# Kernel optimization log

Hardware: AMD Instinct MI355X
Metric: run time of the kernel (lower is better)

Reference implementation:

```python
import jax, jax.numpy as jnp
import numpy as np

N, E = 50000, 800000
IN, HID, HEADS, OUT = 128, 32, 8, 40
D1 = HID * HEADS  # 256


def setup_inputs() -> dict:
    key = jax.random.key(0)
    ks = jax.random.split(key, 24)

    def w(k, fin, fout):
        return (jax.random.normal(k, (fin, fout), jnp.float32) / np.sqrt(fin)).astype(jnp.float32)

    def b(k, fout):
        return (jax.random.normal(k, (fout,), jnp.float32) * 0.02).astype(jnp.float32)

    inp = {
        "x": jax.random.normal(ks[0], (N, IN), jnp.float32),
        "edge_index": jax.random.randint(ks[1], (2, E), 0, N, dtype=jnp.int64),
        # layer 1: TransformerConv(IN -> HID, heads=HEADS, concat=True, beta=True)
        "q1w": w(ks[2], IN, D1), "q1b": b(ks[3], D1),
        "k1w": w(ks[4], IN, D1), "k1b": b(ks[5], D1),
        "v1w": w(ks[6], IN, D1), "v1b": b(ks[7], D1),
        "s1w": w(ks[8], IN, D1), "s1b": b(ks[9], D1),
        "b1w": w(ks[10], 3 * D1, 1),
        # layer 2: TransformerConv(D1 -> OUT, heads=1, concat=False, beta=True)
        "q2w": w(ks[11], D1, OUT), "q2b": b(ks[12], OUT),
        "k2w": w(ks[13], D1, OUT), "k2b": b(ks[14], OUT),
        "v2w": w(ks[15], D1, OUT), "v2b": b(ks[16], OUT),
        "s2w": w(ks[17], D1, OUT), "s2b": b(ks[18], OUT),
        "b2w": w(ks[19], 3 * OUT, 1),
    }
    return inp


def _tconv(x, src, dst, qw, qb, kw, kb, vw, vb, sw, sb, bw, heads, ch, concat):
    """PyG TransformerConv (no edge_attr, root_weight=True, beta=True), eval mode."""
    n = x.shape[0]
    q = (x @ qw + qb).reshape(n, heads, ch)
    k = (x @ kw + kb).reshape(n, heads, ch)
    v = (x @ vw + vb).reshape(n, heads, ch)
    # per-edge attention logits: message flows src(j) -> dst(i)
    alpha = jnp.einsum("ehc,ehc->eh", q[dst], k[src]) / np.sqrt(ch)  # [E,H]
    # segment softmax over incoming edges of each dst node
    amax = jax.ops.segment_max(alpha, dst, num_segments=n)  # [N,H]
    a = jnp.exp(alpha - amax[dst])
    asum = jax.ops.segment_sum(a, dst, num_segments=n)  # [N,H]
    attn = a / asum[dst]  # [E,H]
    # scatter-aggregate weighted values
    out = jax.ops.segment_sum(v[src] * attn[:, :, None], dst, num_segments=n)  # [N,H,C]
    out = out.reshape(n, heads * ch) if concat else out.mean(axis=1)
    skip = x @ sw + sb
    beta = jax.nn.sigmoid(jnp.concatenate([out, skip, out - skip], axis=-1) @ bw)  # [N,1]
    return beta * skip + (1.0 - beta) * out


def reference(x, edge_index, q1w, q1b, k1w, k1b, v1w, v1b, s1w, s1b, b1w,
              q2w, q2b, k2w, k2b, v2w, v2b, s2w, s2b, b2w):
    src, dst = edge_index[0], edge_index[1]
    h = jax.nn.elu(_tconv(x, src, dst, q1w, q1b, k1w, k1b, v1w, v1b, s1w, s1b, b1w, HEADS, HID, True))
    return _tconv(h, src, dst, q2w, q2b, k2w, k2b, v2w, v2b, s2w, s2b, b2w, 1, OUT, False)
```

## Files before the change

### kernel.cpp

```cpp
#include <hip/hip_runtime.h>
#include <cstdint>
#include <cstddef>

#define N_NODES 50000
#define N_EDGES 800000
#define IN_F    128
#define HID     32
#define HEADS   8
#define OUT_F   40
#define D1      256
#define W1COLS  1024
#define W2COLS  160
#define CAP     64

typedef unsigned short ushortT;
typedef unsigned char  ucharT;
typedef unsigned short ushortx8 __attribute__((ext_vector_type(8)));
typedef __bf16 bf16x8 __attribute__((ext_vector_type(8)));
typedef float floatx4 __attribute__((ext_vector_type(4)));
typedef float floatx2 __attribute__((ext_vector_type(2)));

__device__ inline ushortT f2bf(float f) {
    union { float f; unsigned int u; } c; c.f = f;
    unsigned int r = c.u + 0x7FFFu + ((c.u >> 16) & 1u);
    return (ushortT)(r >> 16);
}
__device__ inline float bf2f(ushortT h) {
    union { unsigned int u; float f; } c; c.u = ((unsigned int)h) << 16; return c.f;
}

#define PREP_FILL_B  3125
#define PREP_CONV_B  6250
#define PREP_W1_B    512
#define PREP_W2_B    160
#define PREP_TOTAL_B (PREP_FILL_B + PREP_CONV_B + PREP_W1_B + PREP_W2_B)

__global__ __launch_bounds__(256) void k_prep(
        const int* __restrict__ ei, int* __restrict__ cursor, int* __restrict__ col,
        const float* __restrict__ x, ushortT* __restrict__ xb,
        const float* __restrict__ q1w, const float* __restrict__ k1w,
        const float* __restrict__ v1w, const float* __restrict__ s1w,
        const float* __restrict__ q1b, const float* __restrict__ k1b,
        const float* __restrict__ v1b, const float* __restrict__ s1b,
        ushortT* __restrict__ W1T, float* __restrict__ b1c,
        const float* __restrict__ q2w, const float* __restrict__ k2w,
        const float* __restrict__ v2w, const float* __restrict__ s2w,
        const float* __restrict__ q2b, const float* __restrict__ k2b,
        const float* __restrict__ v2b, const float* __restrict__ s2b,
        ushortT* __restrict__ W2T, float* __restrict__ b2c) {
    int b = blockIdx.x;
    int tid = threadIdx.x;
    if (b < PREP_FILL_B) {
        int e = b * 256 + tid;
        if (e < N_EDGES) {
            int d = ei[N_EDGES + e];
            int p = atomicAdd(&cursor[d], 1);
            col[d * CAP + p] = ei[e];
        }
    } else if (b < PREP_FILL_B + PREP_CONV_B) {
        int i = (b - PREP_FILL_B) * 256 + tid;
        float4 v = reinterpret_cast<const float4*>(x)[i];
        ushort4 o;
        o.x = f2bf(v.x); o.y = f2bf(v.y); o.z = f2bf(v.z); o.w = f2bf(v.w);
        reinterpret_cast<ushort4*>(xb)[i] = o;
    } else if (b < PREP_FILL_B + PREP_CONV_B + PREP_W1_B) {
        int t = (b - PREP_FILL_B - PREP_CONV_B) * 256 + tid;
        int c = t / IN_F, k = t % IN_F;
        int sel = c >> 8, cc = c & 255;
        const float* w = sel == 0 ? q1w : sel == 1 ? k1w : sel == 2 ? v1w : s1w;
        W1T[(size_t)c * IN_F + k] = f2bf(w[(size_t)k * D1 + cc]);
        if (k == 0) {
            const float* bb = sel == 0 ? q1b : sel == 1 ? k1b : sel == 2 ? v1b : s1b;
            b1c[c] = bb[cc];
        }
    } else {
        int t = (b - PREP_FILL_B - PREP_CONV_B - PREP_W1_B) * 256 + tid;
        int c = t / D1, k = t % D1;
        int sel = c / OUT_F, cc = c % OUT_F;
        const float* w = sel == 0 ? q2w : sel == 1 ? k2w : sel == 2 ? v2w : s2w;
        W2T[(size_t)c * D1 + k] = f2bf(w[(size_t)k * OUT_F + cc]);
        if (k == 0) {
            const float* bb = sel == 0 ? q2b : sel == 1 ? k2b : sel == 2 ? v2b : s2b;
            b2c[c] = bb[cc];
        }
    }
}

template<int MODE>
__global__ __launch_bounds__(256) void gemm_mfma_pack(
        const ushortT* __restrict__ A, const ushortT* __restrict__ BT,
        const float* __restrict__ bias, float* __restrict__ QSf,
        ushortT* __restrict__ QSh, ucharT* __restrict__ KV8,
        ushortT* __restrict__ K2V2, int M, int K, int Nn) {
    constexpr int TM = 128, TN = 128, TK = 64, LDP = 72;
    __shared__ ushortT As[TM * LDP];
    __shared__ ushortT Bs[TN * LDP];
    int tid = threadIdx.x;
    int lane = tid & 63, wave = tid >> 6;
    int bm = blockIdx.x * TM, bn = blockIdx.y * TN;
    int wm = (wave & 1) * 64, wn = (wave >> 1) * 64;
    int mrow = lane & 15, g = lane >> 4;
    floatx4 acc[4][4] = {};

    for (int k0 = 0; k0 < K; k0 += TK) {
#pragma unroll
        for (int it = 0; it < 4; ++it) {
            int idx = tid + it * 256;
            int r = idx >> 3, c = (idx & 7) * 8;
            int gm = bm + r;
            ushortx8 val;
            if (gm < M) val = *reinterpret_cast<const ushortx8*>(A + (size_t)gm * K + k0 + c);
            else        val = (ushortx8)0;
            *reinterpret_cast<ushortx8*>(As + r * LDP + c) = val;
        }
#pragma unroll
        for (int it = 0; it < 4; ++it) {
            int idx = tid + it * 256;
            int r = idx >> 3, c = (idx & 7) * 8;
            int gn = bn + r;
            ushortx8 val;
            if (gn < Nn) val = *reinterpret_cast<const ushortx8*>(BT + (size_t)gn * K + k0 + c);
            else         val = (ushortx8)0;
            *reinterpret_cast<ushortx8*>(Bs + r * LDP + c) = val;
        }
        __syncthreads();
#pragma unroll
        for (int kc = 0; kc < TK / 32; ++kc) {
            bf16x8 a[4], b[4];
#pragma unroll
            for (int i = 0; i < 4; ++i)
                a[i] = *reinterpret_cast<const bf16x8*>(As + (wm + i * 16 + mrow) * LDP + kc * 32 + g * 8);
#pragma unroll
            for (int j = 0; j < 4; ++j)
                b[j] = *reinterpret_cast<const bf16x8*>(Bs + (wn + j * 16 + mrow) * LDP + kc * 32 + g * 8);
#pragma unroll
            for (int i = 0; i < 4; ++i)
#pragma unroll
                for (int j = 0; j < 4; ++j)
                    acc[i][j] = __builtin_amdgcn_mfma_f32_16x16x32_bf16(a[i], b[j], acc[i][j], 0, 0, 0);
        }
        __syncthreads();
    }

    if (MODE == 1) {
        float* lds = reinterpret_cast<float*>(As) + wave * 1088;
        int sec = blockIdx.y >> 1;
        int ccbase = (blockIdx.y & 1) * 128 + wn;
        int cb4 = (lane & 15) * 4;
        int rlo = lane >> 4;
        float4 bv = *reinterpret_cast<const float4*>(bias + blockIdx.y * 128 + wn + cb4);
#pragma unroll
        for (int i = 0; i < 4; ++i) {
#pragma unroll
            for (int j = 0; j < 4; ++j)
#pragma unroll
                for (int r = 0; r < 4; ++r)
                    lds[(g * 4 + r) * 68 + j * 16 + mrow] = acc[i][j][r];
#pragma unroll
            for (int it = 0; it < 4; ++it) {
                int row = it * 4 + rlo;
                int gm = bm + wm + i * 16 + row;
                if (gm >= M) continue;
                float4 v = *reinterpret_cast<float4*>(lds + row * 68 + cb4);
                v.x += bv.x; v.y += bv.y; v.z += bv.z; v.w += bv.w;
                int cc = ccbase + cb4;
                if (sec == 0 || sec == 3) {
                    ushort4 h;
                    h.x = f2bf(v.x); h.y = f2bf(v.y); h.z = f2bf(v.z); h.w = f2bf(v.w);
                    ushortT* dst = QSh + (size_t)gm * 512 + (sec == 3 ? 256 : 0) + cc;
                    *reinterpret_cast<ushort4*>(dst) = h;
                } else {
                    unsigned int pk = 0;
                    pk = __builtin_amdgcn_cvt_pk_fp8_f32(v.x, v.y, pk, false);
                    pk = __builtin_amdgcn_cvt_pk_fp8_f32(v.z, v.w, pk, true);
                    ucharT* dst = KV8 + (size_t)gm * 512 + (sec == 2 ? 256 : 0) + cc;
                    *reinterpret_cast<unsigned int*>(dst) = pk;
                }
            }
        }
    } else {
#pragma unroll
        for (int i = 0; i < 4; ++i) {
#pragma unroll
            for (int j = 0; j < 4; ++j) {
                int gn = bn + wn + j * 16 + mrow;
                if (gn >= Nn) continue;
                float bvs = bias[gn];
#pragma unroll
                for (int r = 0; r < 4; ++r) {
                    int gm = bm + wm + i * 16 + g * 4 + r;
                    if (gm >= M) continue;
                    float val = acc[i][j][r] + bvs;
                    int sec = gn / OUT_F, cc = gn % OUT_F;
                    if (sec == 0)      QSf[(size_t)gm * 80 + cc] = val;
                    else if (sec == 1) K2V2[(size_t)gm * 80 + cc] = f2bf(val);
                    else if (sec == 2) K2V2[(size_t)gm * 80 + 40 + cc] = f2bf(val);
                    else               QSf[(size_t)gm * 80 + 40 + cc] = val;
                }
            }
        }
    }
}

__global__ __launch_bounds__(256) void k_edge1(
        const ushortT* __restrict__ QSh, const ucharT* __restrict__ KV8,
        const float* __restrict__ bw,
        const int* __restrict__ degc, const int* __restrict__ col,
        ushortT* __restrict__ H1b) {
    int gid  = blockIdx.x * blockDim.x + threadIdx.x;
    int node = gid >> 6;
    int lane = threadIdx.x & 63;
    if (node >= N_NODES) return;
    const float scale = 0.17677669529663687f;
    ushort4 qh = *reinterpret_cast<const ushort4*>(QSh + (size_t)node * 512 + lane * 4);
    float4 q;
    q.x = bf2f(qh.x) * scale; q.y = bf2f(qh.y) * scale;
    q.z = bf2f(qh.z) * scale; q.w = bf2f(qh.w) * scale;

    float l = 0.f;
    float4 acc = make_float4(0.f, 0.f, 0.f, 0.f);
    int start = node * CAP;
    int d = degc[node];
    int t = 0;
    for (; t + 2 <= d; t += 2) {
        int j0 = col[start + t];
        int j1 = col[start + t + 1];
        const ucharT* row0 = KV8 + (size_t)j0 * 512 + lane * 4;
        const ucharT* row1 = KV8 + (size_t)j1 * 512 + lane * 4;
        unsigned int ku0 = *reinterpret_cast<const unsigned int*>(row0);
        unsigned int vu0 = *reinterpret_cast<const unsigned int*>(row0 + 256);
        unsigned int ku1 = *reinterpret_cast<const unsigned int*>(row1);
        unsigned int vu1 = *reinterpret_cast<const unsigned int*>(row1 + 256);
        floatx2 k0a = __builtin_amdgcn_cvt_pk_f32_fp8(ku0, false);
        floatx2 k0b = __builtin_amdgcn_cvt_pk_f32_fp8(ku0, true);
        floatx2 k1a = __builtin_amdgcn_cvt_pk_f32_fp8(ku1, false);
        floatx2 k1b = __builtin_amdgcn_cvt_pk_f32_fp8(ku1, true);
        float p0 = q.x * k0a[0] + q.y * k0a[1] + q.z * k0b[0] + q.w * k0b[1];
        float p1 = q.x * k1a[0] + q.y * k1a[1] + q.z * k1b[0] + q.w * k1b[1];
        p0 += __shfl_xor(p0, 1);  p1 += __shfl_xor(p1, 1);
        p0 += __shfl_xor(p0, 2);  p1 += __shfl_xor(p1, 2);
        p0 += __shfl_xor(p0, 4);  p1 += __shfl_xor(p1, 4);
        float e0 = __expf(p0);
        float e1 = __expf(p1);
        l += e0 + e1;
        floatx2 v0a = __builtin_amdgcn_cvt_pk_f32_fp8(vu0, false);
        floatx2 v0b = __builtin_amdgcn_cvt_pk_f32_fp8(vu0, true);
        floatx2 v1a = __builtin_amdgcn_cvt_pk_f32_fp8(vu1, false);
        floatx2 v1b = __builtin_amdgcn_cvt_pk_f32_fp8(vu1, true);
        acc.x += e0 * v0a[0] + e1 * v1a[0];
        acc.y += e0 * v0a[1] + e1 * v1a[1];
        acc.z += e0 * v0b[0] + e1 * v1b[0];
        acc.w += e0 * v0b[1] + e1 * v1b[1];
    }
    if (t < d) {
        int j = col[start + t];
        const ucharT* row = KV8 + (size_t)j * 512 + lane * 4;
        unsigned int ku = *reinterpret_cast<const unsigned int*>(row);
        unsigned int vu = *reinterpret_cast<const unsigned int*>(row + 256);
        floatx2 ka = __builtin_amdgcn_cvt_pk_f32_fp8(ku, false);
        floatx2 kb = __builtin_amdgcn_cvt_pk_f32_fp8(ku, true);
        float p0 = q.x * ka[0] + q.y * ka[1] + q.z * kb[0] + q.w * kb[1];
        p0 += __shfl_xor(p0, 1);
        p0 += __shfl_xor(p0, 2);
        p0 += __shfl_xor(p0, 4);
        float e0 = __expf(p0);
        l += e0;
        floatx2 va = __builtin_amdgcn_cvt_pk_f32_fp8(vu, false);
        floatx2 vb = __builtin_amdgcn_cvt_pk_f32_fp8(vu, true);
        acc.x += e0 * va[0];
        acc.y += e0 * va[1];
        acc.z += e0 * vb[0];
        acc.w += e0 * vb[1];
    }
    float inv = (l > 0.f) ? 1.f / l : 0.f;
    float4 o = make_float4(acc.x * inv, acc.y * inv, acc.z * inv, acc.w * inv);
    ushort4 sh = *reinterpret_cast<const ushort4*>(QSh + (size_t)node * 512 + 256 + lane * 4);
    float4 sk;
    sk.x = bf2f(sh.x); sk.y = bf2f(sh.y); sk.z = bf2f(sh.z); sk.w = bf2f(sh.w);
    const int c4 = lane * 4;
    float4 w0 = *reinterpret_cast<const float4*>(bw + c4);
    float4 w1 = *reinterpret_cast<const float4*>(bw + D1 + c4);
    float4 w2 = *reinterpret_cast<const float4*>(bw + 2 * D1 + c4);
    float part = o.x * w0.x + o.y * w0.y + o.z * w0.z + o.w * w0.w
               + sk.x * w1.x + sk.y * w1.y + sk.z * w1.z + sk.w * w1.w
               + (o.x - sk.x) * w2.x + (o.y - sk.y) * w2.y
               + (o.z - sk.z) * w2.z + (o.w - sk.w) * w2.w;
#pragma unroll
    for (int s = 1; s < 64; s <<= 1) part += __shfl_xor(part, s);
    float beta = 1.f / (1.f + __expf(-part));
    float4 h;
    h.x = beta * sk.x + (1.f - beta) * o.x;
    h.y = beta * sk.y + (1.f - beta) * o.y;
    h.z = beta * sk.z + (1.f - beta) * o.z;
    h.w = beta * sk.w + (1.f - beta) * o.w;
    h.x = h.x > 0.f ? h.x : __expf(h.x) - 1.f;
    h.y = h.y > 0.f ? h.y : __expf(h.y) - 1.f;
    h.z = h.z > 0.f ? h.z : __expf(h.z) - 1.f;
    h.w = h.w > 0.f ? h.w : __expf(h.w) - 1.f;
    ushort4 hb;
    hb.x = f2bf(h.x); hb.y = f2bf(h.y); hb.z = f2bf(h.z); hb.w = f2bf(h.w);
    *reinterpret_cast<ushort4*>(H1b + (size_t)node * D1 + c4) = hb;
}

__global__ __launch_bounds__(256) void k_edge2(
        const float* __restrict__ QS, const ushortT* __restrict__ K2V2,
        const float* __restrict__ bw,
        const int* __restrict__ degc, const int* __restrict__ col,
        float* __restrict__ out) {
    __shared__ float        qbuf[4][40];
    __shared__ float        attn[4][64];
    __shared__ int          jb[4][64];
    __shared__ unsigned int ksm[4][64 * 21];
    int gid  = blockIdx.x * blockDim.x + threadIdx.x;
    int node = gid >> 6;
    int wave = threadIdx.x >> 6;
    int lane = threadIdx.x & 63;
    if (node >= N_NODES) return;
    const float scale = 0.15811388300841897f;
    bool act = lane < OUT_F;
    if (act) qbuf[wave][lane] = QS[(size_t)node * 80 + lane] * scale;

    int d = degc[node];
    if (lane < d) jb[wave][lane] = col[node * CAP + lane];

    const unsigned int* Kdw = reinterpret_cast<const unsigned int*>(K2V2);
    int sr = lane / 20;
    int sc = lane - sr * 20;
    for (int r0 = 0; r0 < d; r0 += 3) {
        int rr = r0 + sr;
        if (lane < 60 && rr < d)
            ksm[wave][rr * 21 + sc] = Kdw[(size_t)jb[wave][rr] * 40 + sc];
    }

    float p = 0.f;
    if (lane < d) {
        float s = 0.f;
#pragma unroll
        for (int c = 0; c < 20; ++c) {
            unsigned int kk = ksm[wave][lane * 21 + c];
            s += qbuf[wave][2 * c]     * bf2f((ushortT)(kk & 0xFFFFu))
               + qbuf[wave][2 * c + 1] * bf2f((ushortT)(kk >> 16));
        }
        p = __expf(s);
    }
    attn[wave][lane] = p;
    float l = p;
#pragma unroll
    for (int s = 1; s < 64; s <<= 1) l += __shfl_xor(l, s);

    float acc = 0.f;
    int ln = act ? lane : 0;
    int e = 0;
    for (; e + 4 <= d; e += 4) {
        int je0 = jb[wave][e],     je1 = jb[wave][e + 1];
        int je2 = jb[wave][e + 2], je3 = jb[wave][e + 3];
        float v0 = bf2f(K2V2[(size_t)je0 * 80 + 40 + ln]);
        float v1 = bf2f(K2V2[(size_t)je1 * 80 + 40 + ln]);
        float v2 = bf2f(K2V2[(size_t)je2 * 80 + 40 + ln]);
        float v3 = bf2f(K2V2[(size_t)je3 * 80 + 40 + ln]);
        acc += (attn[wave][e] * v0 + attn[wave][e + 1] * v1)
             + (attn[wave][e + 2] * v2 + attn[wave][e + 3] * v3);
    }
    for (; e < d; ++e)
        acc += attn[wave][e] * bf2f(K2V2[(size_t)jb[wave][e] * 80 + 40 + ln]);

    float inv = (l > 0.f) ? 1.f / l : 0.f;
    float o  = acc * inv;
    float sk = act ? QS[(size_t)node * 80 + 40 + lane] : 0.f;
    float part = act ? (o * bw[lane] + sk * bw[OUT_F + lane] + (o - sk) * bw[2 * OUT_F + lane]) : 0.f;
#pragma unroll
    for (int s = 1; s < 64; s <<= 1) part += __shfl_xor(part, s);
    float beta = 1.f / (1.f + __expf(-part));
    if (act) out[(size_t)node * OUT_F + lane] = beta * sk + (1.f - beta) * o;
}

extern "C" void kernel_launch(void* const* d_in, const int* in_sizes, int n_in,
                              void* d_out, int out_size, void* d_ws, size_t ws_size,
                              hipStream_t stream) {
    const float* x   = (const float*)d_in[0];
    const int*   ei  = (const int*)d_in[1];
    const float* q1w = (const float*)d_in[2];
    const float* q1b = (const float*)d_in[3];
    const float* k1w = (const float*)d_in[4];
    const float* k1b = (const float*)d_in[5];
    const float* v1w = (const float*)d_in[6];
    const float* v1b = (const float*)d_in[7];
    const float* s1w = (const float*)d_in[8];
    const float* s1b = (const float*)d_in[9];
    const float* b1w = (const float*)d_in[10];
    const float* q2w = (const float*)d_in[11];
    const float* q2b = (const float*)d_in[12];
    const float* k2w = (const float*)d_in[13];
    const float* k2b = (const float*)d_in[14];
    const float* v2w = (const float*)d_in[15];
    const float* v2b = (const float*)d_in[16];
    const float* s2w = (const float*)d_in[17];
    const float* s2b = (const float*)d_in[18];
    const float* b2w = (const float*)d_in[19];
    float* out = (float*)d_out;

    char* w = (char*)d_ws;
    ushortT* QSh = (ushortT*)w;
    ucharT*  KV8 = (ucharT*)(w + 51200000);
    ushortT* H1b = (ushortT*)(w + 102400000);
    ushortT* xb  = (ushortT*)(w + 128000000);
    ushortT* W1T = (ushortT*)(w + 140800000);
    ushortT* W2T = (ushortT*)(w + 141062144);
    float*   b1c = (float*)(w + 141144064);
    float*   b2c = (float*)(w + 141148160);
    int* cursor  = (int*)(w + 141149184);
    int* col     = cursor + N_NODES;
    float*   QS2  = (float*)w;
    ushortT* K2V2 = (ushortT*)(w + 51200000);

    hipMemsetAsync(cursor, 0, (size_t)N_NODES * sizeof(int), stream);

    k_prep<<<PREP_TOTAL_B, 256, 0, stream>>>(
        ei, cursor, col, x, xb,
        q1w, k1w, v1w, s1w, q1b, k1b, v1b, s1b, W1T, b1c,
        q2w, k2w, v2w, s2w, q2b, k2b, v2b, s2b, W2T, b2c);

    dim3 g1((N_NODES + 127) / 128, W1COLS / 128);
    gemm_mfma_pack<1><<<g1, 256, 0, stream>>>(xb, W1T, b1c, nullptr, QSh, KV8,
                                              nullptr, N_NODES, IN_F, W1COLS);

    k_edge1<<<(N_NODES * 64) / 256, 256, 0, stream>>>(QSh, KV8, b1w, cursor, col, H1b);

    dim3 g2((N_NODES + 127) / 128, (W2COLS + 127) / 128);
    gemm_mfma_pack<2><<<g2, 256, 0, stream>>>(H1b, W2T, b2c, QS2, nullptr, nullptr,
                                              K2V2, N_NODES, D1, W2COLS);

    k_edge2<<<(N_NODES * 64) / 256, 256, 0, stream>>>(QS2, K2V2, b2w, cursor, col, out);
}
```

Before: 381.6 us.

## Move edge CSR fill into layer-1 GEMM launch, interleaved with GEMM blocks

Moves the atomic-scatter edge bucketing out of the prep kernel and into the first GEMM launch as extra blocks. Fill and GEMM blocks are interleaved so the latency-bound atomic work can overlap with MFMA compute instead of running beforehand. The fill only has to finish before the edge kernel, which still holds. The cost is a flattened 1D grid with index remapping, and shared-memory-heavy GEMM blocks now compete with the fill blocks for occupancy.

```diff
diff --git a/kernel.cpp b/kernel.cpp
--- a/kernel.cpp
+++ b/kernel.cpp
@@ -13,6 +13,12 @@
 #define W2COLS  160
 #define CAP     64
 
+#define GFILL_B   3125
+#define G1_BX     391
+#define G1_BY     8
+#define G1_GEMM_B (G1_BX * G1_BY)
+#define G1_TOTAL  (GFILL_B + G1_GEMM_B)
+
 typedef unsigned short ushortT;
 typedef unsigned char  ucharT;
 typedef unsigned short ushortx8 __attribute__((ext_vector_type(8)));
@@ -29,14 +35,12 @@
     union { unsigned int u; float f; } c; c.u = ((unsigned int)h) << 16; return c.f;
 }
 
-#define PREP_FILL_B  3125
 #define PREP_CONV_B  6250
 #define PREP_W1_B    512
 #define PREP_W2_B    160
-#define PREP_TOTAL_B (PREP_FILL_B + PREP_CONV_B + PREP_W1_B + PREP_W2_B)
+#define PREP_TOTAL_B (PREP_CONV_B + PREP_W1_B + PREP_W2_B)
 
 __global__ __launch_bounds__(256) void k_prep(
-        const int* __restrict__ ei, int* __restrict__ cursor, int* __restrict__ col,
         const float* __restrict__ x, ushortT* __restrict__ xb,
         const float* __restrict__ q1w, const float* __restrict__ k1w,
         const float* __restrict__ v1w, const float* __restrict__ s1w,
@@ -50,21 +54,14 @@
         ushortT* __restrict__ W2T, float* __restrict__ b2c) {
     int b = blockIdx.x;
     int tid = threadIdx.x;
-    if (b < PREP_FILL_B) {
-        int e = b * 256 + tid;
-        if (e < N_EDGES) {
-            int d = ei[N_EDGES + e];
-            int p = atomicAdd(&cursor[d], 1);
-            col[d * CAP + p] = ei[e];
-        }
-    } else if (b < PREP_FILL_B + PREP_CONV_B) {
-        int i = (b - PREP_FILL_B) * 256 + tid;
+    if (b < PREP_CONV_B) {
+        int i = b * 256 + tid;
         float4 v = reinterpret_cast<const float4*>(x)[i];
         ushort4 o;
         o.x = f2bf(v.x); o.y = f2bf(v.y); o.z = f2bf(v.z); o.w = f2bf(v.w);
         reinterpret_cast<ushort4*>(xb)[i] = o;
-    } else if (b < PREP_FILL_B + PREP_CONV_B + PREP_W1_B) {
-        int t = (b - PREP_FILL_B - PREP_CONV_B) * 256 + tid;
+    } else if (b < PREP_CONV_B + PREP_W1_B) {
+        int t = (b - PREP_CONV_B) * 256 + tid;
         int c = t / IN_F, k = t % IN_F;
         int sel = c >> 8, cc = c & 255;
         const float* w = sel == 0 ? q1w : sel == 1 ? k1w : sel == 2 ? v1w : s1w;
@@ -74,7 +71,7 @@
             b1c[c] = bb[cc];
         }
     } else {
-        int t = (b - PREP_FILL_B - PREP_CONV_B - PREP_W1_B) * 256 + tid;
+        int t = (b - PREP_CONV_B - PREP_W1_B) * 256 + tid;
         int c = t / D1, k = t % D1;
         int sel = c / OUT_F, cc = c % OUT_F;
         const float* w = sel == 0 ? q2w : sel == 1 ? k2w : sel == 2 ? v2w : s2w;
@@ -91,13 +88,37 @@
         const ushortT* __restrict__ A, const ushortT* __restrict__ BT,
         const float* __restrict__ bias, float* __restrict__ QSf,
         ushortT* __restrict__ QSh, ucharT* __restrict__ KV8,
-        ushortT* __restrict__ K2V2, int M, int K, int Nn) {
+        ushortT* __restrict__ K2V2,
+        const int* __restrict__ ei, int* __restrict__ cursor, int* __restrict__ col,
+        int M, int K, int Nn) {
     constexpr int TM = 128, TN = 128, TK = 64, LDP = 72;
     __shared__ ushortT As[TM * LDP];
     __shared__ ushortT Bs[TN * LDP];
+    int bx2, by2;
+    if (MODE == 1) {
+        int t = blockIdx.x;
+        int idx;
+        bool isFill;
+        if (t < 2 * GFILL_B) { isFill = !(t & 1); idx = t >> 1; }
+        else                 { isFill = false;    idx = t - GFILL_B; }
+        if (isFill) {
+            int e = idx * 256 + threadIdx.x;
+            if (e < N_EDGES) {
+                int dd = ei[N_EDGES + e];
+                int p = atomicAdd(&cursor[dd], 1);
+                col[dd * CAP + p] = ei[e];
+            }
+            return;
+        }
+        bx2 = idx % G1_BX;
+        by2 = idx / G1_BX;
+    } else {
+        bx2 = blockIdx.x;
+        by2 = blockIdx.y;
+    }
     int tid = threadIdx.x;
     int lane = tid & 63, wave = tid >> 6;
-    int bm = blockIdx.x * TM, bn = blockIdx.y * TN;
+    int bm = bx2 * TM, bn = by2 * TN;
     int wm = (wave & 1) * 64, wn = (wave >> 1) * 64;
     int mrow = lane & 15, g = lane >> 4;
     floatx4 acc[4][4] = {};
@@ -144,11 +165,11 @@
 
     if (MODE == 1) {
         float* lds = reinterpret_cast<float*>(As) + wave * 1088;
-        int sec = blockIdx.y >> 1;
-        int ccbase = (blockIdx.y & 1) * 128 + wn;
+        int sec = by2 >> 1;
+        int ccbase = (by2 & 1) * 128 + wn;
         int cb4 = (lane & 15) * 4;
         int rlo = lane >> 4;
-        float4 bv = *reinterpret_cast<const float4*>(bias + blockIdx.y * 128 + wn + cb4);
+        float4 bv = *reinterpret_cast<const float4*>(bias + by2 * 128 + wn + cb4);
 #pragma unroll
         for (int i = 0; i < 4; ++i) {
 #pragma unroll
@@ -416,19 +437,20 @@
     hipMemsetAsync(cursor, 0, (size_t)N_NODES * sizeof(int), stream);
 
     k_prep<<<PREP_TOTAL_B, 256, 0, stream>>>(
-        ei, cursor, col, x, xb,
+        x, xb,
         q1w, k1w, v1w, s1w, q1b, k1b, v1b, s1b, W1T, b1c,
         q2w, k2w, v2w, s2w, q2b, k2b, v2b, s2b, W2T, b2c);
 
-    dim3 g1((N_NODES + 127) / 128, W1COLS / 128);
-    gemm_mfma_pack<1><<<g1, 256, 0, stream>>>(xb, W1T, b1c, nullptr, QSh, KV8,
-                                              nullptr, N_NODES, IN_F, W1COLS);
+    gemm_mfma_pack<1><<<G1_TOTAL, 256, 0, stream>>>(
+        xb, W1T, b1c, nullptr, QSh, KV8, nullptr,
+        ei, cursor, col, N_NODES, IN_F, W1COLS);
 
     k_edge1<<<(N_NODES * 64) / 256, 256, 0, stream>>>(QSh, KV8, b1w, cursor, col, H1b);
 
     dim3 g2((N_NODES + 127) / 128, (W2COLS + 127) / 128);
     gemm_mfma_pack<2><<<g2, 256, 0, stream>>>(H1b, W2T, b2c, QS2, nullptr, nullptr,
-                                              K2V2, N_NODES, D1, W2COLS);
+                                              K2V2, nullptr, nullptr, nullptr,
+                                              N_NODES, D1, W2COLS);
 
     k_edge2<<<(N_NODES * 64) / 256, 256, 0, stream>>>(QS2, K2V2, b2w, cursor, col, out);
 }
```

Measured after the change: 376.3 us. Within noise of the previous version (-1.4%).
